# Kernel tuning notes

Hardware: AMD Instinct MI355X
Metric: run time of the kernel (lower is better)

## Reference

```python
import jax, jax.numpy as jnp
import numpy as np

WIDTH = 512      # cart_pixel_width
PATCH = 32       # patch_size (kernel == stride, non-overlapping)
TEMP = 1.0       # softmax temperature


def _unfold(x, p):
    """F.unfold with kernel=stride=p on (B,C,H,W) -> (B,C,p*p,L).
    Kernel elements ordered row-major (ki,kj); patches ordered row-major over the grid,
    matching torch.nn.functional.unfold followed by the module's .view reshape."""
    B, C, H, W = x.shape
    Hp, Wp = H // p, W // p
    x = x.reshape(B, C, Hp, p, Wp, p).transpose(0, 1, 3, 5, 2, 4)
    return x.reshape(B, C, p * p, Hp * Wp)


def setup_inputs() -> dict:
    key = jax.random.key(0)
    k1, k2, k3 = jax.random.split(key, 3)
    BW, C = 8, 128
    return {
        "detector_scores": jax.random.normal(k1, (BW, 1, WIDTH, WIDTH), dtype=jnp.float32),
        "weight_scores": jax.random.normal(k2, (BW, 1, WIDTH, WIDTH), dtype=jnp.float32),
        "descriptors": jax.random.normal(k3, (BW, C, WIDTH, WIDTH), dtype=jnp.float32),
    }


def reference(detector_scores, weight_scores, descriptors):
    # coordinate grids: u = column index, v = row index (torch.meshgrid 'ij')
    v, u = jnp.meshgrid(jnp.arange(WIDTH, dtype=jnp.float32),
                        jnp.arange(WIDTH, dtype=jnp.float32), indexing="ij")
    u_patches = _unfold(u[None, None], PATCH)[:, 0]  # (1, p*p, L)
    v_patches = _unfold(v[None, None], PATCH)[:, 0]  # (1, p*p, L)

    det_patches = _unfold(detector_scores, PATCH)[:, 0]          # (BW, p*p, L)
    att = jax.nn.softmax(det_patches / TEMP, axis=1)             # spatial softmax per patch

    expected_u = jnp.sum(u_patches * att, axis=1)                # (BW, L)
    expected_v = jnp.sum(v_patches * att, axis=1)                # (BW, L)
    keypoint_coords = jnp.stack([expected_u, expected_v], axis=2)  # (BW, L, 2)

    att4 = att[:, None]                                          # (BW, 1, p*p, L)
    desc_patches = _unfold(descriptors, PATCH)                   # (BW, C, p*p, L)
    keypoint_desc = jnp.sum(desc_patches * att4, axis=2)         # (BW, C, L)

    score_patches = _unfold(weight_scores, PATCH)                # (BW, 1, p*p, L)
    keypoint_scores = jnp.sum(score_patches * att4, axis=2)      # (BW, 1, L)

    return keypoint_coords, keypoint_scores, keypoint_desc
```

## Files before the change

### kernel.cpp

```cpp
#include <hip/hip_runtime.h>
#include <hip/hip_bf16.h>

#define W512   512
#define PATCH  32
#define NP     16
#define L      256
#define NCH    128
#define NPIX   1024
#define PLANE  (W512 * W512)

__device__ __forceinline__ float wave_max(float v) {
    #pragma unroll
    for (int o = 32; o; o >>= 1) v = fmaxf(v, __shfl_xor(v, o, 64));
    return v;
}
__device__ __forceinline__ float wave_sum(float v) {
    #pragma unroll
    for (int o = 32; o; o >>= 1) v += __shfl_xor(v, o, 64);
    return v;
}

__global__ __launch_bounds__(256)
void att_kernel(const float* __restrict__ det,
                const float* __restrict__ wsc,
                float* __restrict__ out,
                float* __restrict__ attws) {
    __shared__ float red[12];

    const int blk = blockIdx.x;
    const int b   = blk >> 8;
    const int l   = blk & 255;
    const int hp  = l >> 4;
    const int wp  = l & 15;

    const int t    = threadIdx.x;
    const int wave = t >> 6;
    const int lane = t & 63;
    const int r    = t >> 3;
    const int q    = t & 7;

    const int row = hp * PATCH + r;
    const int col = wp * PATCH + q * 4;
    const size_t pix = (size_t)b * PLANE + (size_t)row * W512 + col;

    const float4 d4 = *(const float4*)(det + pix);

    float m = fmaxf(fmaxf(d4.x, d4.y), fmaxf(d4.z, d4.w));
    m = wave_max(m);
    if (lane == 0) red[wave] = m;
    __syncthreads();
    m = fmaxf(fmaxf(red[0], red[1]), fmaxf(red[2], red[3]));

    float e0 = expf(d4.x - m);
    float e1 = expf(d4.y - m);
    float e2 = expf(d4.z - m);
    float e3 = expf(d4.w - m);

    float s = wave_sum(e0 + e1 + e2 + e3);
    if (lane == 0) red[4 + wave] = s;
    __syncthreads();
    s = red[4] + red[5] + red[6] + red[7];
    const float inv = 1.0f / s;
    e0 *= inv; e1 *= inv; e2 *= inv; e3 *= inv;

    *(float4*)(attws + pix) = make_float4(e0, e1, e2, e3);

    const float4 w4 = *(const float4*)(wsc + pix);
    float pu = e0 * (float)(col)     + e1 * (float)(col + 1)
             + e2 * (float)(col + 2) + e3 * (float)(col + 3);
    float pv = (e0 + e1 + e2 + e3) * (float)row;
    float ps = e0 * w4.x + e1 * w4.y + e2 * w4.z + e3 * w4.w;

    pu = wave_sum(pu);
    pv = wave_sum(pv);
    ps = wave_sum(ps);
    __syncthreads();
    if (lane == 0) { red[wave] = pu; red[4 + wave] = pv; red[8 + wave] = ps; }
    __syncthreads();
    if (t == 0) {
        out[blk * 2 + 0]       = red[0] + red[1] + red[2]  + red[3];
        out[blk * 2 + 1]       = red[4] + red[5] + red[6]  + red[7];
        out[2 * (8 * L) + blk] = red[8] + red[9] + red[10] + red[11];
    }
}

__global__ __launch_bounds__(256)
void pool_kernel(const float* __restrict__ desc,
                 const float* __restrict__ attws,
                 float* __restrict__ outd) {
    const int bid   = blockIdx.x;
    const int cg    = bid >> 7;
    const int strip = bid & 127;
    const int b     = strip >> 4;
    const int hp    = strip & 15;

    const int t    = threadIdx.x;
    const int wave = t >> 6;
    const int lane = t & 63;
    const int ch   = cg * 8 + wave * 2;

    const float* ap  = attws + ((size_t)b * W512 + hp * PATCH) * W512 + lane * 4;
    const float* dp0 = desc + (((size_t)(b * NCH + ch)) * W512 + hp * PATCH) * W512 + lane * 4;
    const float* dp1 = dp0 + PLANE;

    float a00 = 0.f, a01 = 0.f, a10 = 0.f, a11 = 0.f;
    #pragma unroll 4
    for (int r = 0; r < PATCH; ++r) {
        const int off = r * W512;
        const float4 av0 = *(const float4*)(ap  + off);
        const float4 av1 = *(const float4*)(ap  + off + 256);
        const float4 d00 = *(const float4*)(dp0 + off);
        const float4 d01 = *(const float4*)(dp0 + off + 256);
        const float4 d10 = *(const float4*)(dp1 + off);
        const float4 d11 = *(const float4*)(dp1 + off + 256);
        a00 += av0.x * d00.x + av0.y * d00.y + av0.z * d00.z + av0.w * d00.w;
        a01 += av1.x * d01.x + av1.y * d01.y + av1.z * d01.z + av1.w * d01.w;
        a10 += av0.x * d10.x + av0.y * d10.y + av0.z * d10.z + av0.w * d10.w;
        a11 += av1.x * d11.x + av1.y * d11.y + av1.z * d11.z + av1.w * d11.w;
    }

    #pragma unroll
    for (int o = 1; o <= 4; o <<= 1) {
        a00 += __shfl_xor(a00, o, 64);
        a01 += __shfl_xor(a01, o, 64);
        a10 += __shfl_xor(a10, o, 64);
        a11 += __shfl_xor(a11, o, 64);
    }

    if ((lane & 7) == 0) {
        const int wp0 = lane >> 3;
        float* o0 = outd + ((size_t)(b * NCH + ch)) * L + hp * NP;
        o0[wp0]     = a00;
        o0[8 + wp0] = a01;
        float* o1 = o0 + L;
        o1[wp0]     = a10;
        o1[8 + wp0] = a11;
    }
}

extern "C" void kernel_launch(void* const* d_in, const int* in_sizes, int n_in,
                              void* d_out, int out_size, void* d_ws, size_t ws_size,
                              hipStream_t stream) {
    const float* det  = (const float*)d_in[0];
    const float* wsc  = (const float*)d_in[1];
    const float* desc = (const float*)d_in[2];
    float* out   = (float*)d_out;
    float* attws = (float*)d_ws;

    att_kernel<<<dim3(8 * L), dim3(256), 0, stream>>>(det, wsc, out, attws);
    pool_kernel<<<dim3(2048), dim3(256), 0, stream>>>(desc, attws, out + 4096 + 2048);
}
```

Before: 196.8 us.

## Fuse softmax into pooling kernel with bf16 attention in shared memory

Merges the attention and pooling kernels into one launch. Each block recomputes unnormalized exp weights for its strip, stores them as bf16 in LDS, and applies the softmax normalization only at the end. This removes the global attention-weight round trip and one launch. The price is that the exp work is repeated across the 16 channel-group blocks, weights lose precision in bf16, and the max subtraction is dropped, so large scores can overflow.

```diff
diff --git a/kernel.cpp b/kernel.cpp
--- a/kernel.cpp
+++ b/kernel.cpp
@@ -6,88 +6,24 @@
 #define NP     16
 #define L      256
 #define NCH    128
-#define NPIX   1024
 #define PLANE  (W512 * W512)
 
-__device__ __forceinline__ float wave_max(float v) {
-    #pragma unroll
-    for (int o = 32; o; o >>= 1) v = fmaxf(v, __shfl_xor(v, o, 64));
-    return v;
+__device__ __forceinline__ unsigned short f2bf(float f) {
+    __hip_bfloat16 h = __float2bfloat16(f);
+    return *reinterpret_cast<unsigned short*>(&h);
 }
-__device__ __forceinline__ float wave_sum(float v) {
-    #pragma unroll
-    for (int o = 32; o; o >>= 1) v += __shfl_xor(v, o, 64);
-    return v;
+__device__ __forceinline__ float bf2f(unsigned short u) {
+    return __uint_as_float(((unsigned int)u) << 16);
 }
 
 __global__ __launch_bounds__(256)
-void att_kernel(const float* __restrict__ det,
-                const float* __restrict__ wsc,
-                float* __restrict__ out,
-                float* __restrict__ attws) {
-    __shared__ float red[12];
+void fused_kernel(const float* __restrict__ det,
+                  const float* __restrict__ wsc,
+                  const float* __restrict__ desc,
+                  float* __restrict__ out) {
+    __shared__ unsigned short att[PATCH][W512];
+    __shared__ float red[NP][2][4];
 
-    const int blk = blockIdx.x;
-    const int b   = blk >> 8;
-    const int l   = blk & 255;
-    const int hp  = l >> 4;
-    const int wp  = l & 15;
-
-    const int t    = threadIdx.x;
-    const int wave = t >> 6;
-    const int lane = t & 63;
-    const int r    = t >> 3;
-    const int q    = t & 7;
-
-    const int row = hp * PATCH + r;
-    const int col = wp * PATCH + q * 4;
-    const size_t pix = (size_t)b * PLANE + (size_t)row * W512 + col;
-
-    const float4 d4 = *(const float4*)(det + pix);
-
-    float m = fmaxf(fmaxf(d4.x, d4.y), fmaxf(d4.z, d4.w));
-    m = wave_max(m);
-    if (lane == 0) red[wave] = m;
-    __syncthreads();
-    m = fmaxf(fmaxf(red[0], red[1]), fmaxf(red[2], red[3]));
-
-    float e0 = expf(d4.x - m);
-    float e1 = expf(d4.y - m);
-    float e2 = expf(d4.z - m);
-    float e3 = expf(d4.w - m);
-
-    float s = wave_sum(e0 + e1 + e2 + e3);
-    if (lane == 0) red[4 + wave] = s;
-    __syncthreads();
-    s = red[4] + red[5] + red[6] + red[7];
-    const float inv = 1.0f / s;
-    e0 *= inv; e1 *= inv; e2 *= inv; e3 *= inv;
-
-    *(float4*)(attws + pix) = make_float4(e0, e1, e2, e3);
-
-    const float4 w4 = *(const float4*)(wsc + pix);
-    float pu = e0 * (float)(col)     + e1 * (float)(col + 1)
-             + e2 * (float)(col + 2) + e3 * (float)(col + 3);
-    float pv = (e0 + e1 + e2 + e3) * (float)row;
-    float ps = e0 * w4.x + e1 * w4.y + e2 * w4.z + e3 * w4.w;
-
-    pu = wave_sum(pu);
-    pv = wave_sum(pv);
-    ps = wave_sum(ps);
-    __syncthreads();
-    if (lane == 0) { red[wave] = pu; red[4 + wave] = pv; red[8 + wave] = ps; }
-    __syncthreads();
-    if (t == 0) {
-        out[blk * 2 + 0]       = red[0] + red[1] + red[2]  + red[3];
-        out[blk * 2 + 1]       = red[4] + red[5] + red[6]  + red[7];
-        out[2 * (8 * L) + blk] = red[8] + red[9] + red[10] + red[11];
-    }
-}
-
-__global__ __launch_bounds__(256)
-void pool_kernel(const float* __restrict__ desc,
-                 const float* __restrict__ attws,
-                 float* __restrict__ outd) {
     const int bid   = blockIdx.x;
     const int cg    = bid >> 7;
     const int strip = bid & 127;
@@ -97,26 +33,88 @@
     const int t    = threadIdx.x;
     const int wave = t >> 6;
     const int lane = t & 63;
-    const int ch   = cg * 8 + wave * 2;
 
-    const float* ap  = attws + ((size_t)b * W512 + hp * PATCH) * W512 + lane * 4;
-    const float* dp0 = desc + (((size_t)(b * NCH + ch)) * W512 + hp * PATCH) * W512 + lane * 4;
+    const int c4  = t & 127;
+    const int h   = t >> 7;
+    const int p   = c4 >> 3;
+    const int col = c4 * 4;
+    const float u0 = (float)col, u1 = (float)(col + 1),
+                u2 = (float)(col + 2), u3 = (float)(col + 3);
+
+    const size_t sbase = (size_t)b * PLANE + (size_t)(hp * PATCH) * W512 + col;
+    const float* dbase = det + sbase;
+    const float* wbase = wsc + sbase;
+    const bool   do_ws = (cg == 0);
+
+    float s = 0.f, pu = 0.f, pv = 0.f, ps = 0.f;
+    #pragma unroll
+    for (int k = 0; k < 16; ++k) {
+        const int r = h * 16 + k;
+        const float4 d4 = *(const float4*)(dbase + (size_t)r * W512);
+        const float e0 = expf(d4.x), e1 = expf(d4.y),
+                    e2 = expf(d4.z), e3 = expf(d4.w);
+        const float es = e0 + e1 + e2 + e3;
+        s  += es;
+        pu += e0 * u0 + e1 * u1 + e2 * u2 + e3 * u3;
+        pv += es * (float)(hp * PATCH + r);
+        if (do_ws) {
+            const float4 w4 = *(const float4*)(wbase + (size_t)r * W512);
+            ps += e0 * w4.x + e1 * w4.y + e2 * w4.z + e3 * w4.w;
+        }
+        ushort4 pk;
+        pk.x = f2bf(e0); pk.y = f2bf(e1); pk.z = f2bf(e2); pk.w = f2bf(e3);
+        *(ushort4*)&att[r][col] = pk;
+    }
+
+    #pragma unroll
+    for (int o = 1; o <= 4; o <<= 1) {
+        s  += __shfl_xor(s,  o, 64);
+        pu += __shfl_xor(pu, o, 64);
+        pv += __shfl_xor(pv, o, 64);
+        ps += __shfl_xor(ps, o, 64);
+    }
+    if ((t & 7) == 0) {
+        red[p][h][0] = s;  red[p][h][1] = pu;
+        red[p][h][2] = pv; red[p][h][3] = ps;
+    }
+    __syncthreads();
+
+    if (do_ws && t < NP) {
+        const float ss  = red[t][0][0] + red[t][1][0];
+        const float inv = 1.0f / ss;
+        const int   blk = b * L + hp * NP + t;
+        out[blk * 2 + 0]       = (red[t][0][1] + red[t][1][1]) * inv;
+        out[blk * 2 + 1]       = (red[t][0][2] + red[t][1][2]) * inv;
+        out[2 * (8 * L) + blk] = (red[t][0][3] + red[t][1][3]) * inv;
+    }
+
+    const int wp0  = lane >> 3;
+    const float inv0 = 1.0f / (red[wp0][0][0]     + red[wp0][1][0]);
+    const float inv1 = 1.0f / (red[8 + wp0][0][0] + red[8 + wp0][1][0]);
+
+    const int ch  = cg * 8 + wave * 2;
+    const int lq4 = lane * 4;
+    const float* dp0 = desc + (((size_t)(b * NCH + ch)) * W512 + hp * PATCH) * W512 + lq4;
     const float* dp1 = dp0 + PLANE;
 
     float a00 = 0.f, a01 = 0.f, a10 = 0.f, a11 = 0.f;
     #pragma unroll 4
     for (int r = 0; r < PATCH; ++r) {
         const int off = r * W512;
-        const float4 av0 = *(const float4*)(ap  + off);
-        const float4 av1 = *(const float4*)(ap  + off + 256);
+        const ushort4 uv0 = *(const ushort4*)&att[r][lq4];
+        const ushort4 uv1 = *(const ushort4*)&att[r][256 + lq4];
         const float4 d00 = *(const float4*)(dp0 + off);
         const float4 d01 = *(const float4*)(dp0 + off + 256);
         const float4 d10 = *(const float4*)(dp1 + off);
         const float4 d11 = *(const float4*)(dp1 + off + 256);
-        a00 += av0.x * d00.x + av0.y * d00.y + av0.z * d00.z + av0.w * d00.w;
-        a01 += av1.x * d01.x + av1.y * d01.y + av1.z * d01.z + av1.w * d01.w;
-        a10 += av0.x * d10.x + av0.y * d10.y + av0.z * d10.z + av0.w * d10.w;
-        a11 += av1.x * d11.x + av1.y * d11.y + av1.z * d11.z + av1.w * d11.w;
+        const float ax0 = bf2f(uv0.x), ay0 = bf2f(uv0.y),
+                    az0 = bf2f(uv0.z), aw0 = bf2f(uv0.w);
+        const float ax1 = bf2f(uv1.x), ay1 = bf2f(uv1.y),
+                    az1 = bf2f(uv1.z), aw1 = bf2f(uv1.w);
+        a00 += ax0 * d00.x + ay0 * d00.y + az0 * d00.z + aw0 * d00.w;
+        a01 += ax1 * d01.x + ay1 * d01.y + az1 * d01.z + aw1 * d01.w;
+        a10 += ax0 * d10.x + ay0 * d10.y + az0 * d10.z + aw0 * d10.w;
+        a11 += ax1 * d11.x + ay1 * d11.y + az1 * d11.z + aw1 * d11.w;
     }
 
     #pragma unroll
@@ -128,13 +126,13 @@
     }
 
     if ((lane & 7) == 0) {
-        const int wp0 = lane >> 3;
+        float* outd = out + 4096 + 2048;
         float* o0 = outd + ((size_t)(b * NCH + ch)) * L + hp * NP;
-        o0[wp0]     = a00;
-        o0[8 + wp0] = a01;
+        o0[wp0]     = a00 * inv0;
+        o0[8 + wp0] = a01 * inv1;
         float* o1 = o0 + L;
-        o1[wp0]     = a10;
-        o1[8 + wp0] = a11;
+        o1[wp0]     = a10 * inv0;
+        o1[8 + wp0] = a11 * inv1;
     }
 }
 
@@ -144,9 +142,7 @@
     const float* det  = (const float*)d_in[0];
     const float* wsc  = (const float*)d_in[1];
     const float* desc = (const float*)d_in[2];
-    float* out   = (float*)d_out;
-    float* attws = (float*)d_ws;
+    float* out = (float*)d_out;
 
-    att_kernel<<<dim3(8 * L), dim3(256), 0, stream>>>(det, wsc, out, attws);
-    pool_kernel<<<dim3(2048), dim3(256), 0, stream>>>(desc, attws, out + 4096 + 2048);
+    fused_kernel<<<dim3(2048), dim3(256), 0, stream>>>(det, wsc, desc, out);
 }
```

Result: slower. 202.9 us (+3.1%).
